# Optimization experiments

Hardware: AMD Instinct MI355X
Metric: run time of the kernel (lower is better)

## Reference

```python
import jax, jax.numpy as jnp
import numpy as np

D = 2048          # hidden_size
I = 8192          # expert_intermediate_size
E = 8             # num_experts
TOP_K = 2
N_CONST = 2       # ConstantExpert count (CONSTANT=2); experts: [copy, zero, ce0, ce1, shared_mlp x (E-4)]


def setup_inputs() -> dict:
    key = jax.random.key(0)
    ks = jax.random.split(key, 9)
    s = 0.02
    return {
        "hidden_states": jax.random.normal(ks[0], (2, 2048, D), dtype=jnp.float32),
        "gate_w1": jax.random.normal(ks[1], (D, E * 8), dtype=jnp.float32) * s,
        "gate_w2": jax.random.normal(ks[2], (E * 8, E), dtype=jnp.float32) * s,
        "ce_wg": jax.random.normal(ks[3], (N_CONST, D, 2), dtype=jnp.float32) * s,
        "ce_const": jax.random.normal(ks[4], (N_CONST, D), dtype=jnp.float32),
        "w_gate": jax.random.normal(ks[5], (D, I), dtype=jnp.float32) * s,
        "w_up": jax.random.normal(ks[6], (D, I), dtype=jnp.float32) * s,
        "w_down": jax.random.normal(ks[7], (I, D), dtype=jnp.float32) * s,
    }


def reference(hidden_states, gate_w1, gate_w2, ce_wg, ce_const, w_gate, w_up, w_down):
    B, S, d = hidden_states.shape
    x = hidden_states.reshape(-1, d).astype(jnp.float32)          # [N, D] tokens

    # Router: MLP gate (fp32) -> softmax -> top-2
    router_logits = jnp.tanh(x @ gate_w1) @ gate_w2               # [N, E]
    probs = jax.nn.softmax(router_logits, axis=-1)
    topw, topi = jax.lax.top_k(probs, TOP_K)                      # [N, 2]
    # mask out last expert (idx == E-1), renormalize
    topw = jnp.where(topi == E - 1, jnp.zeros_like(topw), topw)
    topw = topw / jnp.sum(topw, axis=-1, keepdims=True)
    # per-expert combined routing weight (top-k indices are distinct)
    pe = jnp.sum(topw[..., None] * jax.nn.one_hot(topi, E, dtype=topw.dtype), axis=1)  # [N, E]

    def const_expert(wg, c):
        cw = jax.nn.softmax(x @ wg, axis=-1)                      # [N, 2]
        return cw[:, :1] * x + cw[:, 1:] * c[None, :]

    # shared SwiGLU expert (all dense experts share the same weights in the source)
    swiglu = (jax.nn.silu(x @ w_gate) * (x @ w_up)) @ w_down      # [N, D]

    out = (pe[:, 0:1] * x                                          # CopyExpert (expert 1 = ZeroExpert contributes 0)
           + pe[:, 2:3] * const_expert(ce_wg[0], ce_const[0])
           + pe[:, 3:4] * const_expert(ce_wg[1], ce_const[1])
           + jnp.sum(pe[:, 4:], axis=1, keepdims=True) * swiglu)   # shared dense experts 4..E-1
    return out.reshape(B, S, d), router_logits
```

## Files before the change

### kernel.cpp

```cpp
#include <hip/hip_runtime.h>
#include <stdint.h>
#include <stddef.h>

#define TOKS 4096
#define DH   2048
#define DI   8192

typedef __attribute__((ext_vector_type(8))) short short8v;
typedef __attribute__((ext_vector_type(4))) short short4v;
typedef __attribute__((ext_vector_type(4))) float floatx4;

__device__ __forceinline__ float b2f(short s) {
  union { unsigned u; float f; } v;
  v.u = ((unsigned)(unsigned short)s) << 16;
  return v.f;
}
__device__ __forceinline__ short f2b(float f) {
  union { float f; unsigned u; } v; v.f = f;
  unsigned r = (v.u + 0x7fffu + ((v.u >> 16) & 1u)) >> 16;
  return (short)(unsigned short)r;
}
__device__ __forceinline__ void gload_lds16(const void* g, void* l) {
  __builtin_amdgcn_global_load_lds((const __attribute__((address_space(1))) void*)g,
                                   (__attribute__((address_space(3))) void*)l, 16, 0, 0);
}

__global__ __launch_bounds__(256) void cvt_f32_to_bf16(const float* __restrict__ in,
                                                       short* __restrict__ out) {
  size_t i = (size_t)blockIdx.x * 256 + threadIdx.x;
  floatx4 v = *(const floatx4*)&in[i * 4];
  short4v o;
  o[0] = f2b(v[0]); o[1] = f2b(v[1]); o[2] = f2b(v[2]); o[3] = f2b(v[3]);
  *(short4v*)&out[i * 4] = o;
}

__global__ __launch_bounds__(256) void transpose_to_bf16(const float* __restrict__ in,
                                                         short* __restrict__ out,
                                                         int K, int N,
                                                         int rstride, int roff) {
  __shared__ float tile[32][33];
  const int n0 = blockIdx.x * 32, k0 = blockIdx.y * 32;
  const int tx = threadIdx.x & 31, ty = threadIdx.x >> 5;
#pragma unroll
  for (int yy = 0; yy < 32; yy += 8)
    tile[ty + yy][tx] = in[(size_t)(k0 + ty + yy) * N + n0 + tx];
  __syncthreads();
#pragma unroll
  for (int yy = 0; yy < 32; yy += 8)
    out[((size_t)(n0 + ty + yy) * rstride + roff) * K + k0 + tx] = f2b(tile[tx][ty + yy]);
}

#define RT_TPB 8
__global__ __launch_bounds__(256) void router_kernel(const float* __restrict__ x,
                                                     const float* __restrict__ gw1,
                                                     const float* __restrict__ gw2,
                                                     const float* __restrict__ cwg,
                                                     float* __restrict__ logits_out,
                                                     float* __restrict__ coef) {
  const int wave = threadIdx.x >> 6, lane = threadIdx.x & 63;
  const int tok0 = blockIdx.x * RT_TPB;
  __shared__ float xs[RT_TPB][512];
  __shared__ float ll[RT_TPB][8];
  __shared__ float cd[RT_TPB][4];

  float tj[2] = {0.f, 0.f};
  float cda[2][4] = {{0.f,0.f,0.f,0.f},{0.f,0.f,0.f,0.f}};

  const int st = threadIdx.x >> 5;
  const int sl = threadIdx.x & 31;

  for (int c = 0; c < 4; ++c) {
    const int dbase = c * 512;
#pragma unroll
    for (int r = 0; r < 4; ++r) {
      const int idx = r * 128 + sl * 4;
      *(floatx4*)&xs[st][idx] = *(const floatx4*)&x[(size_t)(tok0 + st) * DH + dbase + idx];
    }
    __syncthreads();
    for (int d = 0; d < 512; ++d) {
      const float g = gw1[(size_t)(dbase + d) * 64 + lane];
      tj[0] += xs[wave * 2 + 0][d] * g;
      tj[1] += xs[wave * 2 + 1][d] * g;
    }
#pragma unroll
    for (int dq = 0; dq < 8; ++dq) {
      const int d = dq * 64 + lane;
      const float w0 = cwg[(size_t)(dbase + d) * 2 + 0];
      const float w1 = cwg[(size_t)(dbase + d) * 2 + 1];
      const float w2 = cwg[(size_t)DH * 2 + (dbase + d) * 2 + 0];
      const float w3 = cwg[(size_t)DH * 2 + (dbase + d) * 2 + 1];
#pragma unroll
      for (int t = 0; t < 2; ++t) {
        const float xv = xs[wave * 2 + t][d];
        cda[t][0] += xv * w0; cda[t][1] += xv * w1;
        cda[t][2] += xv * w2; cda[t][3] += xv * w3;
      }
    }
    __syncthreads();
  }

#pragma unroll
  for (int t = 0; t < 2; ++t) {
    const float th = tanhf(tj[t]);
#pragma unroll
    for (int e = 0; e < 8; ++e) {
      float p = th * gw2[lane * 8 + e];
      for (int off = 32; off; off >>= 1) p += __shfl_xor(p, off);
      if (lane == 0) ll[wave * 2 + t][e] = p;
    }
#pragma unroll
    for (int dd = 0; dd < 4; ++dd) {
      float p = cda[t][dd];
      for (int off = 32; off; off >>= 1) p += __shfl_xor(p, off);
      if (lane == 0) cd[wave * 2 + t][dd] = p;
    }
  }
  __syncthreads();

  if (threadIdx.x < RT_TPB) {
    const int t = threadIdx.x;
    const int gtok = tok0 + t;
    float l[8];
#pragma unroll
    for (int e = 0; e < 8; ++e) l[e] = ll[t][e];
#pragma unroll
    for (int e = 0; e < 8; ++e) logits_out[(size_t)gtok * 8 + e] = l[e];
    float m = l[0];
#pragma unroll
    for (int e = 1; e < 8; ++e) m = fmaxf(m, l[e]);
    float p[8], s = 0.f;
#pragma unroll
    for (int e = 0; e < 8; ++e) { p[e] = expf(l[e] - m); s += p[e]; }
#pragma unroll
    for (int e = 0; e < 8; ++e) p[e] /= s;
    int i1 = 0;
#pragma unroll
    for (int e = 1; e < 8; ++e) if (p[e] > p[i1]) i1 = e;
    int i2 = -1;
#pragma unroll
    for (int e = 0; e < 8; ++e) {
      if (e == i1) continue;
      if (i2 < 0 || p[e] > p[i2]) i2 = e;
    }
    float w1 = (i1 == 7) ? 0.f : p[i1];
    float w2 = (i2 == 7) ? 0.f : p[i2];
    const float nrm = w1 + w2;
    w1 /= nrm; w2 /= nrm;
    float pe[8];
#pragma unroll
    for (int e = 0; e < 8; ++e) pe[e] = 0.f;
    pe[i1] += w1; pe[i2] += w2;
    const float cw00 = 1.f / (1.f + expf(cd[t][1] - cd[t][0]));
    const float cw10 = 1.f / (1.f + expf(cd[t][3] - cd[t][2]));
    coef[gtok * 4 + 0] = pe[0] + pe[2] * cw00 + pe[3] * cw10;
    coef[gtok * 4 + 1] = pe[2] * (1.f - cw00);
    coef[gtok * 4 + 2] = pe[3] * (1.f - cw10);
    coef[gtok * 4 + 3] = pe[4] + pe[5] + pe[6] + pe[7];
  }
}

__device__ __forceinline__ void gemm_mainloop(const short* __restrict__ A,
                                              const short* __restrict__ Bt,
                                              int K, int lda, int ldb,
                                              int m0, int n0,
                                              short* As, short* Bs,
                                              floatx4 (&acc)[4][4]) {
  const int wave = threadIdx.x >> 6;
  const int lane = threadIdx.x & 63;
  const int srow = lane >> 3;
  const int scol = ((lane & 7) ^ srow) * 8;
  const int wm = (wave & 1) * 64;
  const int wn = (wave >> 1) * 64;
  const int l15 = lane & 15;
  const int quad = lane >> 4;
  const int q0 = ((quad ^ (l15 & 7)) * 8);

  for (int k0 = 0; k0 < K; k0 += 64) {
#pragma unroll
    for (int q = 0; q < 4; ++q) {
      const int chunk = wave * 4 + q;
      const int row = chunk * 8 + srow;
      gload_lds16(A + (size_t)(m0 + row) * lda + k0 + scol, &As[chunk * 8 * 64]);
      gload_lds16(Bt + (size_t)(n0 + row) * ldb + k0 + scol, &Bs[chunk * 8 * 64]);
    }
    __syncthreads();
#pragma unroll
    for (int kk = 0; kk < 2; ++kk) {
      const int qo = q0 ^ (kk * 32);
      short8v af[4], bf[4];
#pragma unroll
      for (int i = 0; i < 4; ++i) {
        af[i] = *(const short8v*)&As[(wm + i * 16 + l15) * 64 + qo];
        bf[i] = *(const short8v*)&Bs[(wn + i * 16 + l15) * 64 + qo];
      }
#pragma unroll
      for (int mi = 0; mi < 4; ++mi)
#pragma unroll
        for (int ni = 0; ni < 4; ++ni)
          acc[mi][ni] = __builtin_amdgcn_mfma_f32_16x16x32_bf16(af[mi], bf[ni],
                                                                acc[mi][ni], 0, 0, 0);
    }
    __syncthreads();
  }
}

__global__ __launch_bounds__(256) void gemm1_gu_silu(const short* __restrict__ A,
                                                     const short* __restrict__ Bt,
                                                     short* __restrict__ H,
                                                     int K, int lda, int ldb) {
  __shared__ short As[128 * 64];
  __shared__ short Bs[128 * 64];
  floatx4 acc[4][4];
#pragma unroll
  for (int a = 0; a < 4; ++a)
#pragma unroll
    for (int b = 0; b < 4; ++b) acc[a][b] = (floatx4)0.0f;
  const int lin = blockIdx.y * gridDim.x + blockIdx.x;
  const int m0 = (lin & 31) * 128, n0 = (lin >> 5) * 128;
  gemm_mainloop(A, Bt, K, lda, ldb, m0, n0, As, Bs, acc);
  const int wave = threadIdx.x >> 6, lane = threadIdx.x & 63;
  const int wm = (wave & 1) * 64, wn = (wave >> 1) * 64;
  const int l15 = lane & 15, q4 = (lane >> 4) * 4;
#pragma unroll
  for (int mi = 0; mi < 4; ++mi) {
    const int row0 = m0 + wm + mi * 16 + q4;
#pragma unroll
    for (int ni = 0; ni < 4; ++ni) {
      const int col = n0 + wn + ni * 16 + l15;
#pragma unroll
      for (int rg = 0; rg < 4; ++rg) {
        const float v = acc[mi][ni][rg];
        const float p = __shfl_xor(v, 1);
        if ((l15 & 1) == 0) {
          const float h = (v / (1.f + __expf(-v))) * p;
          H[(size_t)(row0 + rg) * DI + (col >> 1)] = f2b(h);
        }
      }
    }
  }
}

__global__ __launch_bounds__(256) void gemm_bt_moe(const short* __restrict__ A,
                                                   const short* __restrict__ Bt,
                                                   float* __restrict__ out,
                                                   const float* __restrict__ x,
                                                   const float* __restrict__ cc,
                                                   const float* __restrict__ coef,
                                                   int K, int lda, int ldb) {
  __shared__ short As[128 * 64];
  __shared__ short Bs[128 * 64];
  floatx4 acc[4][4];
#pragma unroll
  for (int a = 0; a < 4; ++a)
#pragma unroll
    for (int b = 0; b < 4; ++b) acc[a][b] = (floatx4)0.0f;
  const int lin = blockIdx.y * gridDim.x + blockIdx.x;
  const int m0 = (lin & 31) * 128, n0 = (lin >> 5) * 128;
  gemm_mainloop(A, Bt, K, lda, ldb, m0, n0, As, Bs, acc);
  const int wave = threadIdx.x >> 6, lane = threadIdx.x & 63;
  const int wm = (wave & 1) * 64, wn = (wave >> 1) * 64;
  const int l15 = lane & 15, q4 = (lane >> 4) * 4;
#pragma unroll
  for (int mi = 0; mi < 4; ++mi) {
    const int row0 = m0 + wm + mi * 16 + q4;
#pragma unroll
    for (int ni = 0; ni < 4; ++ni) {
      const int col = n0 + wn + ni * 16 + l15;
      const float c0v = cc[col];
      const float c1v = cc[DH + col];
#pragma unroll
      for (int rg = 0; rg < 4; ++rg) {
        const int row = row0 + rg;
        const floatx4 cf = *(const floatx4*)&coef[row * 4];
        out[(size_t)row * DH + col] =
            cf[0] * x[(size_t)row * DH + col] + cf[1] * c0v + cf[2] * c1v +
            cf[3] * acc[mi][ni][rg];
      }
    }
  }
}

extern "C" void kernel_launch(void* const* d_in, const int* in_sizes, int n_in,
                              void* d_out, int out_size, void* d_ws, size_t ws_size,
                              hipStream_t stream) {
  const float* x   = (const float*)d_in[0];
  const float* gw1 = (const float*)d_in[1];
  const float* gw2 = (const float*)d_in[2];
  const float* cwg = (const float*)d_in[3];
  const float* cc  = (const float*)d_in[4];
  const float* wg  = (const float*)d_in[5];
  const float* wu  = (const float*)d_in[6];
  const float* wd  = (const float*)d_in[7];
  float* out = (float*)d_out;
  float* logits_out = out + (size_t)TOKS * DH;

  char* ws = (char*)d_ws;
  short* xb    = (short*)(ws);
  short* wgwuT = (short*)(ws + 16777216);
  short* wdT   = (short*)(ws + 16777216 + 67108864);
  short* H     = (short*)(ws + 117440512);
  float* coef  = (float*)(ws + 117440512 + 67108864);

  cvt_f32_to_bf16<<<(TOKS * DH) / (256 * 4), 256, 0, stream>>>(x, xb);
  transpose_to_bf16<<<dim3(DI / 32, DH / 32), 256, 0, stream>>>(wg, wgwuT, DH, DI, 2, 0);
  transpose_to_bf16<<<dim3(DI / 32, DH / 32), 256, 0, stream>>>(wu, wgwuT, DH, DI, 2, 1);
  transpose_to_bf16<<<dim3(DH / 32, DI / 32), 256, 0, stream>>>(wd, wdT, DI, DH, 1, 0);
  router_kernel<<<TOKS / RT_TPB, 256, 0, stream>>>(x, gw1, gw2, cwg, logits_out, coef);
  gemm1_gu_silu<<<dim3((2 * DI) / 128, TOKS / 128), 256, 0, stream>>>(
      xb, wgwuT, H, DH, DH, DH);
  gemm_bt_moe<<<dim3(DH / 128, TOKS / 128), 256, 0, stream>>>(
      H, wdT, out, x, cc, coef, DI, DI, DI);
}
```

Baseline: 862.1 us.

## Rewrite gate/up GEMM as 256x256 double-buffered 8-wave pipelined kernel

Replaces the 128x128 single-buffered gate/up GEMM with a 256x256-tile, 512-thread kernel. It double-buffers LDS, interleaves async global-to-LDS loads with quarter-tile MFMA phases, and uses setprio and explicit waitcnt/barrier scheduling. Workgroups are remapped for XCD locality. The goal is to hide memory latency and raise data reuse per tile in the dominant GEMM, at the cost of much higher LDS and register use and hand-tuned wait counts that must be correct.

Result: no change. 845.3 us (-1.9%).

```diff
diff --git a/kernel.cpp b/kernel.cpp
--- a/kernel.cpp
+++ b/kernel.cpp
@@ -156,6 +156,146 @@
     coef[gtok * 4 + 1] = pe[2] * (1.f - cw00);
     coef[gtok * 4 + 2] = pe[3] * (1.f - cw10);
     coef[gtok * 4 + 3] = pe[4] + pe[5] + pe[6] + pe[7];
+  }
+}
+
+__global__ __launch_bounds__(512, 2) void gemm1_gu_silu(const short* __restrict__ A,
+                                                        const short* __restrict__ Bt,
+                                                        short* __restrict__ H,
+                                                        int K, int lda, int ldb) {
+  __shared__ __align__(16) short As[2][256 * 64];
+  __shared__ __align__(16) short Bs[2][256 * 64];
+
+  const int wave = threadIdx.x >> 6;
+  const int lane = threadIdx.x & 63;
+  const int wm64 = (wave >> 2) * 64;
+  const int wn32 = (wave & 3) * 32;
+  const int l15 = lane & 15;
+  const int quad = lane >> 4;
+  const int rq = l15 & 7;
+  const int qoff0 = (quad ^ rq) * 8;
+  const int qoff1 = ((4 + quad) ^ rq) * 8;
+
+  const int srow = lane >> 3;
+  const int scol = ((lane & 7) ^ srow) * 8;
+
+  const int cpx = gridDim.x >> 3;
+  const int wg = ((int)blockIdx.x & 7) * cpx + ((int)blockIdx.x >> 3);
+  const int m0 = (wg & 15) * 256;
+  const int n0 = (wg >> 4) * 256;
+
+  const short* pA = A + (size_t)(m0 + wave * 16 + srow) * lda + scol;
+  const short* pB = Bt + (size_t)(n0 + wave * 16 + srow) * ldb + scol;
+
+  floatx4 acc[8][4];
+#pragma unroll
+  for (int i = 0; i < 8; ++i)
+#pragma unroll
+    for (int j = 0; j < 4; ++j) acc[i][j] = (floatx4)0.f;
+
+  short8v a[4][2];
+  short8v b[4][2];
+
+#define STAGE_A(buf, half, k0)                                                  \
+  {                                                                             \
+    _Pragma("unroll") for (int g = 0; g < 2; ++g)                               \
+        gload_lds16(pA + (size_t)((half) * 128 + g * 8) * lda + (k0),           \
+                    &As[buf][((half) * 128 + wave * 16 + g * 8) * 64]);         \
+  }
+#define STAGE_B(buf, half, k0)                                                  \
+  {                                                                             \
+    _Pragma("unroll") for (int g = 0; g < 2; ++g)                               \
+        gload_lds16(pB + (size_t)((half) * 128 + g * 8) * ldb + (k0),           \
+                    &Bs[buf][((half) * 128 + wave * 16 + g * 8) * 64]);         \
+  }
+#define READ_A(buf, half)                                                       \
+  {                                                                             \
+    _Pragma("unroll") for (int mi = 0; mi < 4; ++mi) {                          \
+      const int r = (half) * 128 + wm64 + mi * 16 + l15;                        \
+      a[mi][0] = *(const short8v*)&As[buf][r * 64 + qoff0];                     \
+      a[mi][1] = *(const short8v*)&As[buf][r * 64 + qoff1];                     \
+    }                                                                           \
+  }
+#define READ_B(buf, half)                                                       \
+  {                                                                             \
+    _Pragma("unroll") for (int ni = 0; ni < 2; ++ni) {                          \
+      const int r = (half) * 128 + wn32 + ni * 16 + l15;                        \
+      b[(half) * 2 + ni][0] = *(const short8v*)&Bs[buf][r * 64 + qoff0];        \
+      b[(half) * 2 + ni][1] = *(const short8v*)&Bs[buf][r * 64 + qoff1];        \
+    }                                                                           \
+  }
+#define MFMA_Q(mh, nh)                                                          \
+  {                                                                             \
+    __builtin_amdgcn_s_setprio(1);                                              \
+    _Pragma("unroll") for (int kk = 0; kk < 2; ++kk)                            \
+    _Pragma("unroll") for (int mi = 0; mi < 4; ++mi)                            \
+    _Pragma("unroll") for (int ni = 0; ni < 2; ++ni)                            \
+        acc[(mh) * 4 + mi][(nh) * 2 + ni] = __builtin_amdgcn_mfma_f32_16x16x32_bf16( \
+            a[mi][kk], b[(nh) * 2 + ni][kk], acc[(mh) * 4 + mi][(nh) * 2 + ni], \
+            0, 0, 0);                                                           \
+    __builtin_amdgcn_s_setprio(0);                                              \
+  }
+#define BAR __builtin_amdgcn_s_barrier()
+#define LGKM0 asm volatile("s_waitcnt lgkmcnt(0)" ::: "memory")
+#define VMC(n) asm volatile("s_waitcnt vmcnt(" #n ")" ::: "memory")
+
+#define KTILE(t, MODE)                                                          \
+  {                                                                             \
+    const int buf = (t) & 1, nbuf = buf ^ 1;                                    \
+    const int k1 = ((t) + 1) * 64, k2 = ((t) + 2) * 64;                         \
+    (void)k1; (void)k2; (void)nbuf;                                             \
+                                                                   \
+    READ_A(buf, 0); READ_B(buf, 0);                                             \
+    if (MODE <= 1) STAGE_B(nbuf, 1, k1);                                        \
+    BAR; LGKM0; MFMA_Q(0, 0); BAR;                                              \
+                                                                   \
+    READ_B(buf, 1);                                                             \
+    if (MODE == 0) STAGE_A(buf, 0, k2);                                         \
+    BAR; LGKM0; MFMA_Q(0, 1); BAR;                                              \
+                                                                   \
+    READ_A(buf, 1);                                                             \
+    if (MODE == 0) STAGE_B(buf, 0, k2);                                         \
+    BAR; LGKM0; MFMA_Q(1, 0); BAR;                                              \
+                                                                   \
+    if (MODE == 0) { STAGE_A(buf, 1, k2); VMC(6); }                             \
+    if (MODE == 1) { VMC(0); }                                                  \
+    BAR; MFMA_Q(1, 1); BAR;                                                     \
+  }
+
+  STAGE_A(0, 0, 0); STAGE_A(0, 1, 0); STAGE_B(0, 0, 0); STAGE_B(0, 1, 0);
+  STAGE_A(1, 0, 64); STAGE_B(1, 0, 64); STAGE_A(1, 1, 64);
+  VMC(6);
+  BAR;
+
+  const int NT = K >> 6;
+  for (int t = 0; t < NT - 2; ++t) KTILE(t, 0);
+  KTILE(NT - 2, 1);
+  KTILE(NT - 1, 2);
+
+#undef KTILE
+#undef STAGE_A
+#undef STAGE_B
+#undef READ_A
+#undef READ_B
+#undef MFMA_Q
+
+  const int q4 = quad * 4;
+#pragma unroll
+  for (int mi = 0; mi < 8; ++mi) {
+    const int row0 = m0 + (mi >> 2) * 128 + wm64 + (mi & 3) * 16 + q4;
+#pragma unroll
+    for (int ni = 0; ni < 4; ++ni) {
+      const int col = n0 + (ni >> 1) * 128 + wn32 + (ni & 1) * 16 + l15;
+#pragma unroll
+      for (int rg = 0; rg < 4; ++rg) {
+        const float v = acc[mi][ni][rg];
+        const float p = __shfl_xor(v, 1);
+        if ((l15 & 1) == 0) {
+          const float hv = (v / (1.f + __expf(-v))) * p;
+          H[(size_t)(row0 + rg) * DI + (col >> 1)] = f2b(hv);
+        }
+      }
+    }
   }
 }
 
@@ -204,42 +344,6 @@
   }
 }
 
-__global__ __launch_bounds__(256) void gemm1_gu_silu(const short* __restrict__ A,
-                                                     const short* __restrict__ Bt,
-                                                     short* __restrict__ H,
-                                                     int K, int lda, int ldb) {
-  __shared__ short As[128 * 64];
-  __shared__ short Bs[128 * 64];
-  floatx4 acc[4][4];
-#pragma unroll
-  for (int a = 0; a < 4; ++a)
-#pragma unroll
-    for (int b = 0; b < 4; ++b) acc[a][b] = (floatx4)0.0f;
-  const int lin = blockIdx.y * gridDim.x + blockIdx.x;
-  const int m0 = (lin & 31) * 128, n0 = (lin >> 5) * 128;
-  gemm_mainloop(A, Bt, K, lda, ldb, m0, n0, As, Bs, acc);
-  const int wave = threadIdx.x >> 6, lane = threadIdx.x & 63;
-  const int wm = (wave & 1) * 64, wn = (wave >> 1) * 64;
-  const int l15 = lane & 15, q4 = (lane >> 4) * 4;
-#pragma unroll
-  for (int mi = 0; mi < 4; ++mi) {
-    const int row0 = m0 + wm + mi * 16 + q4;
-#pragma unroll
-    for (int ni = 0; ni < 4; ++ni) {
-      const int col = n0 + wn + ni * 16 + l15;
-#pragma unroll
-      for (int rg = 0; rg < 4; ++rg) {
-        const float v = acc[mi][ni][rg];
-        const float p = __shfl_xor(v, 1);
-        if ((l15 & 1) == 0) {
-          const float h = (v / (1.f + __expf(-v))) * p;
-          H[(size_t)(row0 + rg) * DI + (col >> 1)] = f2b(h);
-        }
-      }
-    }
-  }
-}
-
 __global__ __launch_bounds__(256) void gemm_bt_moe(const short* __restrict__ A,
                                                    const short* __restrict__ Bt,
                                                    float* __restrict__ out,
@@ -306,7 +410,7 @@
   transpose_to_bf16<<<dim3(DI / 32, DH / 32), 256, 0, stream>>>(wu, wgwuT, DH, DI, 2, 1);
   transpose_to_bf16<<<dim3(DH / 32, DI / 32), 256, 0, stream>>>(wd, wdT, DI, DH, 1, 0);
   router_kernel<<<TOKS / RT_TPB, 256, 0, stream>>>(x, gw1, gw2, cwg, logits_out, coef);
-  gemm1_gu_silu<<<dim3((2 * DI) / 128, TOKS / 128), 256, 0, stream>>>(
+  gemm1_gu_silu<<<dim3((TOKS / 256) * ((2 * DI) / 256)), 512, 0, stream>>>(
       xb, wgwuT, H, DH, DH, DH);
   gemm_bt_moe<<<dim3(DH / 128, TOKS / 128), 256, 0, stream>>>(
       H, wdT, out, x, cc, coef, DI, DI, DI);
```
